# Kernel tuning notes

Measured on AMD Instinct MI355X. Metric: run time of the kernel, lower is better.

The kernel has to match this reference:

```python
import jax, jax.numpy as jnp
import numpy as np

N = 10000      # nodes
E = 160000     # edges (before self-loops)
IN = 256       # input feature dim
H = 8          # heads
C1, C2, C3 = 64, 128, 256  # per-head out channels per layer
NEG_SLOPE = 0.2


def setup_inputs() -> dict:
    key = jax.random.key(0)
    ks = jax.random.split(key, 16)
    def glorot(k, shape):
        fan_in = shape[-1]
        return jax.random.normal(k, shape, dtype=jnp.float32) * (1.0 / np.sqrt(fan_in))
    x = jax.random.normal(ks[0], (N, IN), dtype=jnp.float32)
    edge_index = jax.random.randint(ks[1], (2, E), 0, N)
    # layer 1: in=IN, out=64 per head, concat
    W1  = glorot(ks[2], (H * C1, IN))
    as1 = glorot(ks[3], (H, C1)); ad1 = glorot(ks[4], (H, C1))
    b1  = jnp.zeros((H * C1,), jnp.float32)
    # layer 2: in=H*C1, out=128 per head, concat
    W2  = glorot(ks[5], (H * C2, H * C1))
    as2 = glorot(ks[6], (H, C2)); ad2 = glorot(ks[7], (H, C2))
    b2  = jnp.zeros((H * C2,), jnp.float32)
    # layer 3: in=H*C2, out=256 per head, mean over heads
    W3  = glorot(ks[8], (H * C3, H * C2))
    as3 = glorot(ks[9], (H, C3)); ad3 = glorot(ks[10], (H, C3))
    b3  = jnp.zeros((C3,), jnp.float32)
    return {"x": x, "edge_index": edge_index,
            "W1": W1, "as1": as1, "ad1": ad1, "b1": b1,
            "W2": W2, "as2": as2, "ad2": ad2, "b2": b2,
            "W3": W3, "as3": as3, "ad3": ad3, "b3": b3}


def gat_layer(x, src, dst, W, a_src, a_dst, b, concat, num_nodes):
    """PyG-style GATConv (inference, dropout off, self-loops already in src/dst)."""
    heads, c = a_src.shape
    h = (x @ W.T).reshape(num_nodes, heads, c)          # [N,H,C]
    alpha_src = (h * a_src).sum(-1)                      # [N,H]
    alpha_dst = (h * a_dst).sum(-1)                      # [N,H]
    e = jax.nn.leaky_relu(alpha_src[src] + alpha_dst[dst], NEG_SLOPE)  # [E,H]
    # segment softmax over edges grouped by destination node
    m = jax.ops.segment_max(e, dst, num_segments=num_nodes)
    m = jnp.where(jnp.isfinite(m), m, 0.0)
    p = jnp.exp(e - m[dst])                              # [E,H]
    s = jax.ops.segment_sum(p, dst, num_segments=num_nodes)
    alpha = p / (s[dst] + 1e-16)                         # [E,H]
    out = jax.ops.segment_sum(alpha[:, :, None] * h[src], dst,
                              num_segments=num_nodes)    # [N,H,C]
    out = out.reshape(num_nodes, heads * c) if concat else out.mean(axis=1)
    return out + b


def reference(x, edge_index, W1, as1, ad1, b1, W2, as2, ad2, b2, W3, as3, ad3, b3):
    n = x.shape[0]
    loop = jnp.arange(n, dtype=edge_index.dtype)         # add_self_loops=True
    src = jnp.concatenate([edge_index[0], loop])
    dst = jnp.concatenate([edge_index[1], loop])
    h = jax.nn.elu(gat_layer(x, src, dst, W1, as1, ad1, b1, True, n))
    h = jax.nn.elu(gat_layer(h, src, dst, W2, as2, ad2, b2, True, n))
    return gat_layer(h, src, dst, W3, as3, ad3, b3, False, n)
```

## Files before the change

### kernel.cpp

```cpp
#include <hip/hip_runtime.h>
#include <cstdint>

#define NNODES 10000
#define NEDGES 160000
#define TOT_E  (NEDGES + NNODES)
#define HEADS  8

typedef unsigned short u16;
typedef __attribute__((ext_vector_type(8))) _Float16 h8;
typedef __attribute__((ext_vector_type(4))) _Float16 h4;
typedef __attribute__((ext_vector_type(4))) float f4;

__device__ inline u16 f2h(float x) {
    union { _Float16 h; u16 u; } c; c.h = (_Float16)x; return c.u;
}

__device__ inline void gld16(const u16* g, u16* l) {
    __builtin_amdgcn_global_load_lds(
        (const __attribute__((address_space(1))) void*)g,
        (__attribute__((address_space(3))) void*)l, 16, 0, 0);
}

__global__ void count_k(const int* __restrict__ ei, int* __restrict__ deg) {
    int i = blockIdx.x * 256 + threadIdx.x;
    if (i >= TOT_E) return;
    int dst = (i < NEDGES) ? ei[NEDGES + i] : (i - NEDGES);
    atomicAdd(deg + dst, 1);
}

__global__ __launch_bounds__(1024) void scan_k(const int* __restrict__ deg,
                                               int* __restrict__ rows) {
    __shared__ int buf[1024];
    int tid = threadIdx.x;
    int base = tid * 10;
    int loc[10]; int s = 0;
    #pragma unroll
    for (int j = 0; j < 10; j++) {
        int i = base + j;
        loc[j] = s;
        s += (i < NNODES) ? deg[i] : 0;
    }
    buf[tid] = s;
    __syncthreads();
    for (int off = 1; off < 1024; off <<= 1) {
        int t = (tid >= off) ? buf[tid - off] : 0;
        __syncthreads();
        buf[tid] += t;
        __syncthreads();
    }
    int ex = tid ? buf[tid - 1] : 0;
    #pragma unroll
    for (int j = 0; j < 10; j++) {
        int i = base + j;
        if (i < NNODES) rows[i] = ex + loc[j];
    }
    if (tid == 1023) rows[NNODES] = buf[1023];
}

__global__ void scatter_k(const int* __restrict__ ei, const int* __restrict__ rows,
                          int* __restrict__ cursor, int* __restrict__ esrc) {
    int i = blockIdx.x * 256 + threadIdx.x;
    if (i >= TOT_E) return;
    int src, dst;
    if (i < NEDGES) { src = ei[i]; dst = ei[NEDGES + i]; }
    else            { src = i - NEDGES; dst = src; }
    int pos = atomicAdd(cursor + dst, 1);
    esrc[rows[dst] + pos] = src;
}

__global__ void cvt16_k(const float* __restrict__ in, u16* __restrict__ o, int n4) {
    int i = blockIdx.x * 256 + threadIdx.x;
    if (i >= n4) return;
    float4 v = ((const float4*)in)[i];
    ushort4 h;
    h.x = f2h(v.x); h.y = f2h(v.y); h.z = f2h(v.z); h.w = f2h(v.w);
    ((ushort4*)o)[i] = h;
}

__global__ __launch_bounds__(256) void gemm_f16(
    const u16* __restrict__ A, const u16* __restrict__ B,
    u16* __restrict__ C16, int M, int N, int K,
    const float* __restrict__ a_s, const float* __restrict__ a_d,
    float* __restrict__ asrc, float* __restrict__ adst, int Chead)
{
    __shared__ u16 sA[8192], sB[8192];
    const int t = threadIdx.x, lane = t & 63, w = t >> 6;
    const int row0 = blockIdx.y * 128, col0 = blockIdx.x * 128;
    const int wm = w & 1, wn = w >> 1;
    const int l15 = lane & 15, quad = lane >> 4;

    const int octg = (lane & 7) ^ (lane >> 3);
    const int rl   = lane >> 3;
    const u16* gp[8]; u16* lp[8];
    #pragma unroll
    for (int q = 0; q < 8; q++) {
        int c = w * 8 + q;
        if (c < 16) {
            int gr = row0 + c * 8 + rl; if (gr >= M) gr = M - 1;
            gp[q] = A + (size_t)gr * K + octg * 8;
            lp[q] = sA + c * 512;
        } else {
            int gc = col0 + (c - 16) * 8 + rl;
            gp[q] = B + (size_t)gc * K + octg * 8;
            lp[q] = sB + (c - 16) * 512;
        }
    }

    const int swz = (l15 & 7);

    f4 acc[4][4];
    #pragma unroll
    for (int i = 0; i < 4; i++)
        #pragma unroll
        for (int j = 0; j < 4; j++)
            acc[i][j] = (f4){0.f, 0.f, 0.f, 0.f};

    for (int k0 = 0; k0 < K; k0 += 64) {
        #pragma unroll
        for (int q = 0; q < 8; q++) {
            gld16(gp[q], lp[q]);
            gp[q] += 64;
        }
        __builtin_amdgcn_s_waitcnt(0);
        __syncthreads();

        #pragma unroll
        for (int s = 0; s < 2; s++) {
            const int po = ((s * 4 + quad) ^ swz) * 8;
            h8 a[4];
            #pragma unroll
            for (int i = 0; i < 4; i++)
                a[i] = *(const h8*)&sA[(wm * 64 + i * 16 + l15) * 64 + po];
            #pragma unroll
            for (int j = 0; j < 4; j++) {
                h8 b = *(const h8*)&sB[(wn * 64 + j * 16 + l15) * 64 + po];
                #pragma unroll
                for (int i = 0; i < 4; i++)
                    acc[i][j] = __builtin_amdgcn_mfma_f32_16x16x32_f16(a[i], b, acc[i][j], 0, 0, 0);
            }
        }
        __syncthreads();
    }

    const int span0 = col0 + wn * 64;
    const int hd = span0 / Chead;
    float av[4], dv[4];
    #pragma unroll
    for (int j = 0; j < 4; j++) {
        av[j] = a_s[span0 + j * 16 + l15];
        dv[j] = a_d[span0 + j * 16 + l15];
    }

    #pragma unroll
    for (int i = 0; i < 4; i++) {
        #pragma unroll
        for (int r = 0; r < 4; r++) {
            int gr = row0 + wm * 64 + i * 16 + quad * 4 + r;
            float s1 = 0.f, s2 = 0.f;
            #pragma unroll
            for (int j = 0; j < 4; j++) {
                float v = acc[i][j][r];
                s1 += v * av[j];
                s2 += v * dv[j];
            }
            #pragma unroll
            for (int m = 1; m < 16; m <<= 1) {
                s1 += __shfl_xor(s1, m);
                s2 += __shfl_xor(s2, m);
            }
            if (gr < M) {
                u16* cp = C16 + (size_t)gr * N + span0 + l15;
                #pragma unroll
                for (int j = 0; j < 4; j++)
                    cp[j * 16] = f2h(acc[i][j][r]);
                if (l15 == 0) {
                    atomicAdd(asrc + gr * HEADS + hd, s1);
                    atomicAdd(adst + gr * HEADS + hd, s2);
                }
            }
        }
    }
}

template<int C, int MODE>
__global__ __launch_bounds__(512) void agg_k(const u16* __restrict__ h16,
                                             const float* __restrict__ asrc,
                                             const float* __restrict__ adst,
                                             const int* __restrict__ rows,
                                             const int* __restrict__ esrc,
                                             const float* __restrict__ bias,
                                             u16* __restrict__ oh,
                                             float* __restrict__ outf) {
    constexpr int LPE = C / 4;
    constexpr int EPW = 64 / LPE;
    constexpr int U   = (LPE == 64) ? 16 : (LPE == 32) ? 12 : 8;
    __shared__ float red[MODE == 1 ? HEADS * 256 : 8];

    const int n    = blockIdx.x;
    const int hd   = threadIdx.x >> 6;
    const int lane = threadIdx.x & 63;
    const int sub  = lane / LPE;
    const int cl   = lane % LPE;
    const int beg = rows[n], end = rows[n + 1], deg = end - beg;
    const float ad = adst[n * HEADS + hd];

    float4 acc = {0.f, 0.f, 0.f, 0.f};

    auto gather = [&](int e, float pw, int cdeg) {
        for (int j = 0; j < cdeg; j += EPW * U) {
            int   sn[U]; float wg[U];
            #pragma unroll
            for (int u = 0; u < U; u++) {
                int idx = j + sub + EPW * u;
                int   ss = __shfl(e, idx);
                float ww = __shfl(pw, idx);
                bool ok = idx < cdeg;
                sn[u] = ok ? ss : 0;
                wg[u] = ok ? ww : 0.f;
            }
            h4 v[U];
            #pragma unroll
            for (int u = 0; u < U; u++)
                v[u] = *(const h4*)(h16 + (size_t)sn[u] * (HEADS * C) + hd * C + cl * 4);
            #pragma unroll
            for (int u = 0; u < U; u++) {
                acc.x += wg[u] * (float)v[u].x; acc.y += wg[u] * (float)v[u].y;
                acc.z += wg[u] * (float)v[u].z; acc.w += wg[u] * (float)v[u].w;
            }
        }
    };

    if (deg <= 64) {
        int e = 0; float p = 0.f;
        if (lane < deg) {
            e = esrc[beg + lane];
            float lg = asrc[e * HEADS + hd] + ad;
            lg = (lg > 0.f) ? lg : 0.2f * lg;
            p = __expf(lg);
        }
        float s = p;
        #pragma unroll
        for (int off = 32; off; off >>= 1) s += __shfl_xor(s, off);
        float pw = p / (s + 1e-16f);
        gather(e, pw, deg);
    } else {
        float ssum = 0.f;
        for (int i = beg + lane; i < end; i += 64) {
            float lg = asrc[esrc[i] * HEADS + hd] + ad;
            lg = (lg > 0.f) ? lg : 0.2f * lg;
            ssum += __expf(lg);
        }
        #pragma unroll
        for (int off = 32; off; off >>= 1) ssum += __shfl_xor(ssum, off);
        float inv = 1.f / (ssum + 1e-16f);
        for (int c0 = beg; c0 < end; c0 += 64) {
            int cdeg = min(64, end - c0);
            int e = 0; float pw = 0.f;
            if (lane < cdeg) {
                e = esrc[c0 + lane];
                float lg = asrc[e * HEADS + hd] + ad;
                lg = (lg > 0.f) ? lg : 0.2f * lg;
                pw = __expf(lg) * inv;
            }
            gather(e, pw, cdeg);
        }
    }

    #pragma unroll
    for (int m = LPE; m < 64; m <<= 1) {
        acc.x += __shfl_xor(acc.x, m); acc.y += __shfl_xor(acc.y, m);
        acc.z += __shfl_xor(acc.z, m); acc.w += __shfl_xor(acc.w, m);
    }

    if constexpr (MODE == 0) {
        if (sub == 0) {
            const float* bp = bias + hd * C + cl * 4;
            float4 b = *(const float4*)bp;
            float r[4] = {acc.x + b.x, acc.y + b.y, acc.z + b.z, acc.w + b.w};
            #pragma unroll
            for (int j = 0; j < 4; j++)
                r[j] = (r[j] > 0.f) ? r[j] : (expf(r[j]) - 1.f);
            ushort4 hv;
            hv.x = f2h(r[0]); hv.y = f2h(r[1]); hv.z = f2h(r[2]); hv.w = f2h(r[3]);
            *(ushort4*)(oh + (size_t)n * (HEADS * C) + hd * C + cl * 4) = hv;
        }
    } else {
        *(float4*)&red[hd * 256 + lane * 4] = acc;
        __syncthreads();
        int tid = threadIdx.x;
        if (tid < 256) {
            float s = 0.f;
            #pragma unroll
            for (int hh = 0; hh < HEADS; hh++) s += red[hh * 256 + tid];
            outf[(size_t)n * 256 + tid] = s * 0.125f + bias[tid];
        }
    }
}

extern "C" void kernel_launch(void* const* d_in, const int* in_sizes, int n_in,
                              void* d_out, int out_size, void* d_ws, size_t ws_size,
                              hipStream_t stream) {
    const float* x   = (const float*)d_in[0];
    const int*   ei  = (const int*)d_in[1];
    const float* W1  = (const float*)d_in[2];
    const float* as1 = (const float*)d_in[3];
    const float* ad1 = (const float*)d_in[4];
    const float* b1  = (const float*)d_in[5];
    const float* W2  = (const float*)d_in[6];
    const float* as2 = (const float*)d_in[7];
    const float* ad2 = (const float*)d_in[8];
    const float* b2  = (const float*)d_in[9];
    const float* W3  = (const float*)d_in[10];
    const float* as3 = (const float*)d_in[11];
    const float* ad3 = (const float*)d_in[12];
    const float* b3  = (const float*)d_in[13];
    float* out = (float*)d_out;

    int* deg    = (int*)d_ws;
    int* cursor = deg + 10240;
    int* rows   = cursor + 10240;
    int* esrc   = rows + 10240;
    float* asrc = (float*)(esrc + 170240);
    float* adst = asrc + 81920;
    u16* Hh     = (u16*)(adst + 81920);
    u16* Af     = Hh + (size_t)NNODES * 2048;
    u16* Wf     = Af + (size_t)NNODES * 1024;

    hipMemsetAsync(deg, 0, 2 * 10240 * sizeof(int), stream);

    count_k<<<(TOT_E + 255) / 256, 256, 0, stream>>>(ei, deg);
    scan_k<<<1, 1024, 0, stream>>>(deg, rows);
    scatter_k<<<(TOT_E + 255) / 256, 256, 0, stream>>>(ei, rows, cursor, esrc);

    const int rowBlocks = (NNODES + 127) / 128;

    cvt16_k<<<(NNODES * 256 / 4 + 255) / 256, 256, 0, stream>>>(x, Af, NNODES * 256 / 4);
    cvt16_k<<<(512 * 256 / 4 + 255) / 256, 256, 0, stream>>>(W1, Wf, 512 * 256 / 4);
    hipMemsetAsync(asrc, 0, 2 * 81920 * sizeof(float), stream);
    gemm_f16<<<dim3(4, rowBlocks), 256, 0, stream>>>(Af, Wf, Hh, NNODES, 512, 256,
                                                     as1, ad1, asrc, adst, 64);
    agg_k<64, 0><<<NNODES, 512, 0, stream>>>(Hh, asrc, adst, rows, esrc, b1, Af, nullptr);

    cvt16_k<<<(1024 * 512 / 4 + 255) / 256, 256, 0, stream>>>(W2, Wf, 1024 * 512 / 4);
    hipMemsetAsync(asrc, 0, 2 * 81920 * sizeof(float), stream);
    gemm_f16<<<dim3(8, rowBlocks), 256, 0, stream>>>(Af, Wf, Hh, NNODES, 1024, 512,
                                                     as2, ad2, asrc, adst, 128);
    agg_k<128, 0><<<NNODES, 512, 0, stream>>>(Hh, asrc, adst, rows, esrc, b2, Af, nullptr);

    cvt16_k<<<(2048 * 1024 / 4 + 255) / 256, 256, 0, stream>>>(W3, Wf, 2048 * 1024 / 4);
    hipMemsetAsync(asrc, 0, 2 * 81920 * sizeof(float), stream);
    gemm_f16<<<dim3(16, rowBlocks), 256, 0, stream>>>(Af, Wf, Hh, NNODES, 2048, 1024,
                                                      as3, ad3, asrc, adst, 256);
    agg_k<256, 1><<<NNODES, 512, 0, stream>>>(Hh, asrc, adst, rows, esrc, b3, nullptr, out);
}
```

Baseline: 473.2 us.

## Pre-swizzle operands into MFMA fragment layout and use LDS-free single-wave GEMM

Input, weight, and aggregated activations are now stored in a tiled layout where each 16x32 MFMA fragment is contiguous, and the aggregation kernel writes its output directly in that layout. This lets a new one-wave GEMM load fragments straight from global memory into registers with 128x128 tiles and double buffering, with no shared memory or barriers. All fp16 conversions are merged into one kernel, and the per-layer memsets collapse into one by giving each layer its own attention-score buffers. The cost is heavy register pressure (64 accumulators plus four fragment arrays) and only 64 threads per block, which may leave latency poorly hidden.

```diff
diff --git a/kernel.cpp b/kernel.cpp
--- a/kernel.cpp
+++ b/kernel.cpp
@@ -5,6 +5,7 @@
 #define NEDGES 160000
 #define TOT_E  (NEDGES + NNODES)
 #define HEADS  8
+#define MT 625
 
 typedef unsigned short u16;
 typedef __attribute__((ext_vector_type(8))) _Float16 h8;
@@ -13,12 +14,6 @@
 
 __device__ inline u16 f2h(float x) {
     union { _Float16 h; u16 u; } c; c.h = (_Float16)x; return c.u;
-}
-
-__device__ inline void gld16(const u16* g, u16* l) {
-    __builtin_amdgcn_global_load_lds(
-        (const __attribute__((address_space(1))) void*)g,
-        (__attribute__((address_space(3))) void*)l, 16, 0, 0);
 }
 
 __global__ void count_k(const int* __restrict__ ei, int* __restrict__ deg) {
@@ -68,114 +63,138 @@
     esrc[rows[dst] + pos] = src;
 }
 
-__global__ void cvt16_k(const float* __restrict__ in, u16* __restrict__ o, int n4) {
-    int i = blockIdx.x * 256 + threadIdx.x;
-    if (i >= n4) return;
-    float4 v = ((const float4*)in)[i];
-    ushort4 h;
-    h.x = f2h(v.x); h.y = f2h(v.y); h.z = f2h(v.z); h.w = f2h(v.w);
-    ((ushort4*)o)[i] = h;
-}
-
-__global__ __launch_bounds__(256) void gemm_f16(
+template<int K, int KT>
+__device__ inline void cvt_seg(const float* __restrict__ in, u16* __restrict__ out, int t) {
+    int lane = t & 63;
+    int tmp  = t >> 6;
+    int tk   = tmp % KT;
+    int tr   = tmp / KT;
+    const float* sp = in + (size_t)(tr * 16 + (lane & 15)) * K + tk * 32 + (lane >> 4) * 8;
+    float4 v0 = *(const float4*)sp;
+    float4 v1 = *(const float4*)(sp + 4);
+    ushort4 h0{f2h(v0.x), f2h(v0.y), f2h(v0.z), f2h(v0.w)};
+    ushort4 h1{f2h(v1.x), f2h(v1.y), f2h(v1.z), f2h(v1.w)};
+    *(ushort4*)(out + (size_t)t * 8)     = h0;
+    *(ushort4*)(out + (size_t)t * 8 + 4) = h1;
+}
+
+__global__ __launch_bounds__(256) void cvtsw_all(const float* __restrict__ x,
+        const float* __restrict__ W1, const float* __restrict__ W2,
+        const float* __restrict__ W3, u16* __restrict__ Axs, u16* __restrict__ W1s,
+        u16* __restrict__ W2s, u16* __restrict__ W3s) {
+    int g = blockIdx.x * 256 + threadIdx.x;
+    if (g < 320000)      cvt_seg<256, 8>(x,  Axs, g);
+    else if (g < 336384) cvt_seg<256, 8>(W1, W1s, g - 320000);
+    else if (g < 401920) cvt_seg<512, 16>(W2, W2s, g - 336384);
+    else                 cvt_seg<1024, 32>(W3, W3s, g - 401920);
+}
+
+template<int CHEAD>
+__global__ __launch_bounds__(64) void gemm_dx(
     const u16* __restrict__ A, const u16* __restrict__ B,
-    u16* __restrict__ C16, int M, int N, int K,
+    u16* __restrict__ C16, int N, int K,
     const float* __restrict__ a_s, const float* __restrict__ a_d,
-    float* __restrict__ asrc, float* __restrict__ adst, int Chead)
+    float* __restrict__ asrc, float* __restrict__ adst)
 {
-    __shared__ u16 sA[8192], sB[8192];
-    const int t = threadIdx.x, lane = t & 63, w = t >> 6;
-    const int row0 = blockIdx.y * 128, col0 = blockIdx.x * 128;
-    const int wm = w & 1, wn = w >> 1;
+    const int lane = threadIdx.x;
     const int l15 = lane & 15, quad = lane >> 4;
-
-    const int octg = (lane & 7) ^ (lane >> 3);
-    const int rl   = lane >> 3;
-    const u16* gp[8]; u16* lp[8];
-    #pragma unroll
-    for (int q = 0; q < 8; q++) {
-        int c = w * 8 + q;
-        if (c < 16) {
-            int gr = row0 + c * 8 + rl; if (gr >= M) gr = M - 1;
-            gp[q] = A + (size_t)gr * K + octg * 8;
-            lp[q] = sA + c * 512;
-        } else {
-            int gc = col0 + (c - 16) * 8 + rl;
-            gp[q] = B + (size_t)gc * K + octg * 8;
-            lp[q] = sB + (c - 16) * 512;
-        }
-    }
-
-    const int swz = (l15 & 7);
-
-    f4 acc[4][4];
-    #pragma unroll
-    for (int i = 0; i < 4; i++)
-        #pragma unroll
-        for (int j = 0; j < 4; j++)
+    const int bx = blockIdx.x, by = blockIdx.y;
+    const int row0 = by * 128, col0 = bx * 128;
+    const int KT = K >> 5;
+    const int lo = lane * 8;
+
+    size_t abase[8], bbase[8];
+    #pragma unroll
+    for (int i = 0; i < 8; i++) {
+        int tr = by * 8 + i; if (tr > MT - 1) tr = MT - 1;
+        abase[i] = (size_t)tr * KT * 512;
+    }
+    #pragma unroll
+    for (int j = 0; j < 8; j++)
+        bbase[j] = (size_t)(bx * 8 + j) * KT * 512;
+
+    f4 acc[8][8];
+    #pragma unroll
+    for (int i = 0; i < 8; i++)
+        #pragma unroll
+        for (int j = 0; j < 8; j++)
             acc[i][j] = (f4){0.f, 0.f, 0.f, 0.f};
 
-    for (int k0 = 0; k0 < K; k0 += 64) {
-        #pragma unroll
-        for (int q = 0; q < 8; q++) {
-            gld16(gp[q], lp[q]);
-            gp[q] += 64;
-        }
-        __builtin_amdgcn_s_waitcnt(0);
-        __syncthreads();
-
-        #pragma unroll
-        for (int s = 0; s < 2; s++) {
-            const int po = ((s * 4 + quad) ^ swz) * 8;
-            h8 a[4];
-            #pragma unroll
-            for (int i = 0; i < 4; i++)
-                a[i] = *(const h8*)&sA[(wm * 64 + i * 16 + l15) * 64 + po];
-            #pragma unroll
-            for (int j = 0; j < 4; j++) {
-                h8 b = *(const h8*)&sB[(wn * 64 + j * 16 + l15) * 64 + po];
+    h8 a0[8], b0[8], a1[8], b1[8];
+    #pragma unroll
+    for (int i = 0; i < 8; i++) {
+        a0[i] = *(const h8*)(A + abase[i] + lo);
+        b0[i] = *(const h8*)(B + bbase[i] + lo);
+    }
+
+    for (int t = 0; t < KT; t += 2) {
+        const int off1 = (t + 1) * 512 + lo;
+        #pragma unroll
+        for (int i = 0; i < 8; i++) {
+            a1[i] = *(const h8*)(A + abase[i] + off1);
+            b1[i] = *(const h8*)(B + bbase[i] + off1);
+        }
+        #pragma unroll
+        for (int j = 0; j < 8; j++)
+            #pragma unroll
+            for (int i = 0; i < 8; i++)
+                acc[i][j] = __builtin_amdgcn_mfma_f32_16x16x32_f16(a0[i], b0[j], acc[i][j], 0, 0, 0);
+        if (t + 2 < KT) {
+            const int off2 = (t + 2) * 512 + lo;
+            #pragma unroll
+            for (int i = 0; i < 8; i++) {
+                a0[i] = *(const h8*)(A + abase[i] + off2);
+                b0[i] = *(const h8*)(B + bbase[i] + off2);
+            }
+        }
+        #pragma unroll
+        for (int j = 0; j < 8; j++)
+            #pragma unroll
+            for (int i = 0; i < 8; i++)
+                acc[i][j] = __builtin_amdgcn_mfma_f32_16x16x32_f16(a1[i], b1[j], acc[i][j], 0, 0, 0);
+    }
+
+    float av[8], dv[8];
+    #pragma unroll
+    for (int j = 0; j < 8; j++) {
+        av[j] = a_s[col0 + j * 16 + l15];
+        dv[j] = a_d[col0 + j * 16 + l15];
+    }
+
+    #pragma unroll
+    for (int i = 0; i < 8; i++) {
+        #pragma unroll
+        for (int r = 0; r < 4; r++) {
+            int gr = row0 + i * 16 + quad * 4 + r;
+            float sA0 = 0.f, sD0 = 0.f, sA1 = 0.f, sD1 = 0.f;
+            #pragma unroll
+            for (int j = 0; j < 8; j++) {
+                float v = acc[i][j][r];
+                if (CHEAD == 64 && j >= 4) { sA1 += v * av[j]; sD1 += v * dv[j]; }
+                else                       { sA0 += v * av[j]; sD0 += v * dv[j]; }
+            }
+            #pragma unroll
+            for (int m = 1; m < 16; m <<= 1) {
+                sA0 += __shfl_xor(sA0, m); sD0 += __shfl_xor(sD0, m);
+                if (CHEAD == 64) { sA1 += __shfl_xor(sA1, m); sD1 += __shfl_xor(sD1, m); }
+            }
+            if (gr < NNODES) {
+                u16* cp = C16 + (size_t)gr * N + col0 + l15;
                 #pragma unroll
-                for (int i = 0; i < 4; i++)
-                    acc[i][j] = __builtin_amdgcn_mfma_f32_16x16x32_f16(a[i], b, acc[i][j], 0, 0, 0);
-            }
-        }
-        __syncthreads();
-    }
-
-    const int span0 = col0 + wn * 64;
-    const int hd = span0 / Chead;
-    float av[4], dv[4];
-    #pragma unroll
-    for (int j = 0; j < 4; j++) {
-        av[j] = a_s[span0 + j * 16 + l15];
-        dv[j] = a_d[span0 + j * 16 + l15];
-    }
-
-    #pragma unroll
-    for (int i = 0; i < 4; i++) {
-        #pragma unroll
-        for (int r = 0; r < 4; r++) {
-            int gr = row0 + wm * 64 + i * 16 + quad * 4 + r;
-            float s1 = 0.f, s2 = 0.f;
-            #pragma unroll
-            for (int j = 0; j < 4; j++) {
-                float v = acc[i][j][r];
-                s1 += v * av[j];
-                s2 += v * dv[j];
-            }
-            #pragma unroll
-            for (int m = 1; m < 16; m <<= 1) {
-                s1 += __shfl_xor(s1, m);
-                s2 += __shfl_xor(s2, m);
-            }
-            if (gr < M) {
-                u16* cp = C16 + (size_t)gr * N + span0 + l15;
-                #pragma unroll
-                for (int j = 0; j < 4; j++)
+                for (int j = 0; j < 8; j++)
                     cp[j * 16] = f2h(acc[i][j][r]);
                 if (l15 == 0) {
-                    atomicAdd(asrc + gr * HEADS + hd, s1);
-                    atomicAdd(adst + gr * HEADS + hd, s2);
+                    if (CHEAD == 64) {
+                        int hd0 = col0 >> 6;
+                        atomicAdd(asrc + gr * HEADS + hd0,     sA0);
+                        atomicAdd(adst + gr * HEADS + hd0,     sD0);
+                        atomicAdd(asrc + gr * HEADS + hd0 + 1, sA1);
+                        atomicAdd(adst + gr * HEADS + hd0 + 1, sD1);
+                    } else {
+                        int hd = col0 / CHEAD;
+                        atomicAdd(asrc + gr * HEADS + hd, sA0);
+                        atomicAdd(adst + gr * HEADS + hd, sD0);
+                    }
                 }
             }
         }
@@ -282,7 +301,13 @@
                 r[j] = (r[j] > 0.f) ? r[j] : (expf(r[j]) - 1.f);
             ushort4 hv;
             hv.x = f2h(r[0]); hv.y = f2h(r[1]); hv.z = f2h(r[2]); hv.w = f2h(r[3]);
-            *(ushort4*)(oh + (size_t)n * (HEADS * C) + hd * C + cl * 4) = hv;
+            constexpr int KTO = (HEADS * C) / 32;
+            int c0 = hd * C + cl * 4;
+            int tr = n >> 4;
+            int tk = c0 >> 5;
+            int ln = ((c0 >> 3) & 3) * 16 + (n & 15);
+            size_t idx = ((size_t)(tr * KTO + tk) * 64 + ln) * 8 + (c0 & 7);
+            *(ushort4*)(oh + idx) = hv;
         }
     } else {
         *(float4*)&red[hd * 256 + lane * 4] = acc;
@@ -316,40 +341,37 @@
     const float* b3  = (const float*)d_in[13];
     float* out = (float*)d_out;
 
-    int* deg    = (int*)d_ws;
-    int* cursor = deg + 10240;
-    int* rows   = cursor + 10240;
-    int* esrc   = rows + 10240;
-    float* asrc = (float*)(esrc + 170240);
-    float* adst = asrc + 81920;
-    u16* Hh     = (u16*)(adst + 81920);
-    u16* Af     = Hh + (size_t)NNODES * 2048;
-    u16* Wf     = Af + (size_t)NNODES * 1024;
-
-    hipMemsetAsync(deg, 0, 2 * 10240 * sizeof(int), stream);
+    int*   deg    = (int*)d_ws;
+    int*   cursor = deg + 10240;
+    float* az     = (float*)(cursor + 10240);
+    float* asrc1 = az,           * adst1 = az + 81920;
+    float* asrc2 = az + 163840,  * adst2 = az + 245760;
+    float* asrc3 = az + 327680,  * adst3 = az + 409600;
+    int*   rows   = (int*)(az + 491520);
+    int*   esrc   = rows + 10240;
+    u16*   Hh     = (u16*)(esrc + 170240);
+    u16*   Af     = Hh + (size_t)NNODES * 2048;
+    u16*   Axs    = Af + (size_t)NNODES * 1024;
+    u16*   W1s    = Axs + (size_t)NNODES * 256;
+    u16*   W2s    = W1s + 512 * 256;
+    u16*   W3s    = W2s + 1024 * 512;
+
+    hipMemsetAsync(d_ws, 0, (size_t)(20480 + 491520) * 4, stream);
 
     count_k<<<(TOT_E + 255) / 256, 256, 0, stream>>>(ei, deg);
     scan_k<<<1, 1024, 0, stream>>>(deg, rows);
     scatter_k<<<(TOT_E + 255) / 256, 256, 0, stream>>>(ei, rows, cursor, esrc);
-
-    const int rowBlocks = (NNODES + 127) / 128;
-
-    cvt16_k<<<(NNODES * 256 / 4 + 255) / 256, 256, 0, stream>>>(x, Af, NNODES * 256 / 4);
-    cvt16_k<<<(512 * 256 / 4 + 255) / 256, 256, 0, stream>>>(W1, Wf, 512 * 256 / 4);
-    hipMemsetAsync(asrc, 0, 2 * 81920 * sizeof(float), stream);
-    gemm_f16<<<dim3(4, rowBlocks), 256, 0, stream>>>(Af, Wf, Hh, NNODES, 512, 256,
-                                                     as1, ad1, asrc, adst, 64);
-    agg_k<64, 0><<<NNODES, 512, 0, stream>>>(Hh, asrc, adst, rows, esrc, b1, Af, nullptr);
-
-    cvt16_k<<<(1024 * 512 / 4 + 255) / 256, 256, 0, stream>>>(W2, Wf, 1024 * 512 / 4);
-    hipMemsetAsync(asrc, 0, 2 * 81920 * sizeof(float), stream);
-    gemm_f16<<<dim3(8, rowBlocks), 256, 0, stream>>>(Af, Wf, Hh, NNODES, 1024, 512,
-                                                     as2, ad2, asrc, adst, 128);
-    agg_k<128, 0><<<NNODES, 512, 0, stream>>>(Hh, asrc, adst, rows, esrc, b2, Af, nullptr);
-
-    cvt16_k<<<(2048 * 1024 / 4 + 255) / 256, 256, 0, stream>>>(W3, Wf, 2048 * 1024 / 4);
-    hipMemsetAsync(asrc, 0, 2 * 81920 * sizeof(float), stream);
-    gemm_f16<<<dim3(16, rowBlocks), 256, 0, stream>>>(Af, Wf, Hh, NNODES, 2048, 1024,
-                                                      as3, ad3, asrc, adst, 256);
-    agg_k<256, 1><<<NNODES, 512, 0, stream>>>(Hh, asrc, adst, rows, esrc, b3, nullptr, out);
-}
+    cvtsw_all<<<2594, 256, 0, stream>>>(x, W1, W2, W3, Axs, W1s, W2s, W3s);
+
+    gemm_dx<64><<<dim3(4, 79), 64, 0, stream>>>(Axs, W1s, Hh, 512, 256,
+                                                as1, ad1, asrc1, adst1);
+    agg_k<64, 0><<<NNODES, 512, 0, stream>>>(Hh, asrc1, adst1, rows, esrc, b1, Af, nullptr);
+
+    gemm_dx<128><<<dim3(8, 79), 64, 0, stream>>>(Af, W2s, Hh, 1024, 512,
+                                                 as2, ad2, asrc2, adst2);
+    agg_k<128, 0><<<NNODES, 512, 0, stream>>>(Hh, asrc2, adst2, rows, esrc, b2, Af, nullptr);
+
+    gemm_dx<256><<<dim3(16, 79), 64, 0, stream>>>(Af, W3s, Hh, 2048, 1024,
+                                                  as3, ad3, asrc3, adst3);
+    agg_k<256, 1><<<NNODES, 512, 0, stream>>>(Hh, asrc3, adst3, rows, esrc, b3, nullptr, out);
+}
```

Measured after the change: 502.5 us. +6.2%, slower.
